# Kernel tuning notes

Hardware: AMD Instinct MI355X
Metric: run time of the kernel (lower is better)

## Reference

```python
import jax, jax.numpy as jnp
import numpy as np
import math

S, B, D, H = 2048, 4, 1024, 16
DH = D // H

def setup_inputs() -> dict:
    key = jax.random.key(0)
    ks = jax.random.split(key, 6)
    x = jax.random.normal(ks[0], (S, B, D), dtype=jnp.float32)
    # causal additive mask (finite large negative for numerical safety)
    i = jnp.arange(S)
    attn_mask = jnp.where(i[None, :] > i[:, None], jnp.float32(-1e9), jnp.float32(0.0))
    beta = jnp.zeros((H,), dtype=jnp.float32)  # per-head log-scale, init 0 -> exp=1
    xav = math.sqrt(6.0 / (D + D))  # xavier_uniform bound
    Wq = jax.random.uniform(ks[1], (D, D), minval=-xav, maxval=xav, dtype=jnp.float32)
    Wk = jax.random.uniform(ks[2], (D, D), minval=-xav, maxval=xav, dtype=jnp.float32)
    Wv = jax.random.uniform(ks[3], (D, D), minval=-xav, maxval=xav, dtype=jnp.float32)
    Wo = jax.random.uniform(ks[4], (D, D), minval=-xav, maxval=xav, dtype=jnp.float32)
    z = jnp.zeros((D,), dtype=jnp.float32)
    return {"x": x, "attn_mask": attn_mask, "beta": beta,
            "Wq": Wq, "bq": z, "Wk": Wk, "bk": z, "Wv": Wv, "bv": z, "Wo": Wo, "bo": z}

def reference(x, attn_mask, beta, Wq, bq, Wk, bk, Wv, bv, Wo, bo):
    s, b, d = x.shape
    h, dh = H, DH
    q = x @ Wq.T + bq  # (s, b, d)
    k = x @ Wk.T + bk
    v = x @ Wv.T + bv
    # attn_sink: append zero key/value token, pad mask with a zero column
    k = jnp.concatenate([k, jnp.zeros((1, b, d), k.dtype)], axis=0)  # (s+1, b, d)
    v = jnp.concatenate([v, jnp.zeros((1, b, d), v.dtype)], axis=0)
    mask = jnp.pad(attn_mask, ((0, 0), (0, 1)))  # (s, s+1)
    t = s + 1
    # split heads: (seq, b, h, dh) -> (b, h, seq, dh)
    qh = q.reshape(s, b, h, dh).transpose(1, 2, 0, 3)
    kh = k.reshape(t, b, h, dh).transpose(1, 2, 0, 3)
    vh = v.reshape(t, b, h, dh).transpose(1, 2, 0, 3)
    scale = (jnp.exp(beta) * math.sqrt(dh))[None, :, None, None]
    qh = qh / scale
    scores = jnp.einsum('bhsd,bhtd->bhst', qh, kh) + mask[None, None]
    w = jax.nn.softmax(scores, axis=-1)
    out = jnp.einsum('bhst,bhtd->bhsd', w, vh)  # (b, h, s, dh)
    out = out.transpose(2, 0, 1, 3).reshape(s, b, d)
    return out @ Wo.T + bo
```

## Files before the change

kernel.cpp:

```cpp
#include <hip/hip_runtime.h>
#include <hip/hip_bf16.h>
#include <math.h>

#define S_LEN   2048
#define BATCH   4
#define DMODEL  1024
#define NHEAD   16
#define DHEAD   64
#define MROWS   (S_LEN * BATCH)

typedef __bf16 bf16;
typedef __bf16 bf16x8 __attribute__((ext_vector_type(8)));
typedef __bf16 bf16x4 __attribute__((ext_vector_type(4)));
typedef short  short4_t __attribute__((ext_vector_type(4)));
typedef float  f32x4  __attribute__((ext_vector_type(4)));

#define LOG2E 1.4426950408889634f

#define AS1C(p) (const __attribute__((address_space(1))) void*)(p)
#define AS3(p)  (__attribute__((address_space(3))) void*)(p)


__global__ __launch_bounds__(256) void cast_bf16(const float* __restrict__ in,
                                                 bf16* __restrict__ out, int n8) {
    int i = blockIdx.x * 256 + threadIdx.x;
    if (i >= n8) return;
    const float4* p = (const float4*)in;
    float4 a = p[i * 2], b = p[i * 2 + 1];
    bf16x8 o;
    o[0] = (bf16)a.x; o[1] = (bf16)a.y; o[2] = (bf16)a.z; o[3] = (bf16)a.w;
    o[4] = (bf16)b.x; o[5] = (bf16)b.y; o[6] = (bf16)b.z; o[7] = (bf16)b.w;
    *(bf16x8*)(out + (size_t)i * 8) = o;
}

__global__ __launch_bounds__(256) void cast3_bf16(const float* __restrict__ w0,
                                                  const float* __restrict__ w1,
                                                  const float* __restrict__ w2,
                                                  bf16* __restrict__ out) {
    const int seg = blockIdx.y;
    const float* in = (seg == 0) ? w0 : (seg == 1) ? w1 : w2;
    int i = blockIdx.x * 256 + threadIdx.x;
    const float4* p = (const float4*)in;
    float4 a = p[i * 2], b = p[i * 2 + 1];
    bf16x8 o;
    o[0] = (bf16)a.x; o[1] = (bf16)a.y; o[2] = (bf16)a.z; o[3] = (bf16)a.w;
    o[4] = (bf16)b.x; o[5] = (bf16)b.y; o[6] = (bf16)b.z; o[7] = (bf16)b.w;
    *(bf16x8*)(out + (size_t)seg * DMODEL * DMODEL + (size_t)i * 8) = o;
}

__global__ __launch_bounds__(256, 2) void qkv_gemm(const bf16* __restrict__ A,
                                                   const bf16* __restrict__ W,
                                                   const float* __restrict__ bq,
                                                   const float* __restrict__ bk,
                                                   const float* __restrict__ bv,
                                                   const float* __restrict__ beta,
                                                   bf16* __restrict__ Qo,
                                                   bf16* __restrict__ Kp,
                                                   bf16* __restrict__ Vp) {
    constexpr int BK = 32;
    constexpr int NTILES = DMODEL / BK;
    __shared__ __align__(16) bf16 sA[3][256 * BK];
    __shared__ __align__(16) bf16 sB[3][128 * BK];

    const int t    = threadIdx.x;
    const int lane = t & 63;
    const int wave = t >> 6;
    const int wr   = wave >> 1;
    const int wc   = wave & 1;
    const int lq   = lane & 15;
    const int lg   = lane >> 4;
    const int bn   = blockIdx.x * 128;
    const int bm   = blockIdx.y * 256;

    const int schunk = (lane & 3) ^ ((lane >> 3) & 3);
    const bf16* ApS = A + (size_t)(bm + wave * 64 + (lane >> 2)) * DMODEL + schunk * 8;
    const bf16* WpS = W + (size_t)(bn + wave * 32 + (lane >> 2)) * DMODEL + schunk * 8;
    const int koff = (lg ^ ((lq >> 1) & 3)) * 8;

    f32x4 acc[8][4] = {};

#define QSTAGE(si_, ko_)                                                                              \
    __builtin_amdgcn_global_load_lds(AS1C(ApS + (ko_)),               AS3(&sA[si_][(wave*64 +  0)*BK]), 16,0,0); \
    __builtin_amdgcn_global_load_lds(AS1C(ApS + 16*DMODEL + (ko_)),   AS3(&sA[si_][(wave*64 + 16)*BK]), 16,0,0); \
    __builtin_amdgcn_global_load_lds(AS1C(ApS + 32*DMODEL + (ko_)),   AS3(&sA[si_][(wave*64 + 32)*BK]), 16,0,0); \
    __builtin_amdgcn_global_load_lds(AS1C(ApS + 48*DMODEL + (ko_)),   AS3(&sA[si_][(wave*64 + 48)*BK]), 16,0,0); \
    __builtin_amdgcn_global_load_lds(AS1C(WpS + (ko_)),               AS3(&sB[si_][(wave*32 +  0)*BK]), 16,0,0); \
    __builtin_amdgcn_global_load_lds(AS1C(WpS + 16*DMODEL + (ko_)),   AS3(&sB[si_][(wave*32 + 16)*BK]), 16,0,0);

    QSTAGE(0, 0)
    QSTAGE(1, BK)
    asm volatile("s_waitcnt vmcnt(6)\n\ts_barrier" ::: "memory");

    int bi = 0, si = 2, st = 2;
    for (int tt = 0; tt < NTILES; ++tt) {
        QSTAGE(si, (size_t)st * BK)
        const bf16* At = sA[bi];
        const bf16* Bt = sB[bi];
        bf16x8 bfr[4];
#pragma unroll
        for (int nt = 0; nt < 4; nt++)
            bfr[nt] = *(const bf16x8*)&Bt[(wc * 64 + nt * 16 + lq) * BK + koff];
        bf16x8 af[4];
#pragma unroll
        for (int mt = 0; mt < 4; mt++)
            af[mt] = *(const bf16x8*)&At[(wr * 128 + mt * 16 + lq) * BK + koff];
        __builtin_amdgcn_s_setprio(1);
#pragma unroll
        for (int mt = 0; mt < 4; mt++)
#pragma unroll
            for (int nt = 0; nt < 4; nt++)
                acc[mt][nt] = __builtin_amdgcn_mfma_f32_16x16x32_bf16(af[mt], bfr[nt], acc[mt][nt], 0, 0, 0);
        __builtin_amdgcn_s_setprio(0);
#pragma unroll
        for (int mt = 0; mt < 4; mt++)
            af[mt] = *(const bf16x8*)&At[(wr * 128 + (mt + 4) * 16 + lq) * BK + koff];
        __builtin_amdgcn_s_setprio(1);
#pragma unroll
        for (int mt = 0; mt < 4; mt++)
#pragma unroll
            for (int nt = 0; nt < 4; nt++)
                acc[mt + 4][nt] = __builtin_amdgcn_mfma_f32_16x16x32_bf16(af[mt], bfr[nt], acc[mt + 4][nt], 0, 0, 0);
        __builtin_amdgcn_s_setprio(0);
        asm volatile("s_waitcnt vmcnt(6)\n\ts_barrier" ::: "memory");
        bi = (bi == 2) ? 0 : bi + 1;
        si = (si == 2) ? 0 : si + 1;
        st = (st == NTILES - 1) ? 0 : st + 1;
    }
#undef QSTAGE

    const int seg = blockIdx.x >> 3;
    const int bnl = (blockIdx.x & 7) * 128;
    const float* bias = (seg == 0) ? bq : (seg == 1) ? bk : bv;

    if (seg == 0) {
#pragma unroll
        for (int nt = 0; nt < 4; nt++) {
            const int col = bnl + wc * 64 + nt * 16 + lq;
            const float bvv = bias[col];
            const float sc = LOG2E / (__expf(beta[col >> 6]) * 8.0f);
#pragma unroll
            for (int mt = 0; mt < 8; mt++) {
                const int row = bm + wr * 128 + mt * 16 + lg * 4;
#pragma unroll
                for (int r = 0; r < 4; r++) {
                    float v = (acc[mt][nt][r] + bvv) * sc;
                    Qo[(size_t)(row + r) * DMODEL + col] = (bf16)v;
                }
            }
        }
    } else {
        bf16* out = (seg == 1) ? Kp : Vp;
#pragma unroll
        for (int mt = 0; mt < 8; mt++) {
            const int F   = bm + wr * 128 + mt * 16;
            const int S0X = F >> 2;
            const int T   = S0X >> 4;
            const int sl  = (S0X & 15) + lg;
#pragma unroll
            for (int nt = 0; nt < 4; nt++) {
                const int col = bnl + wc * 64 + nt * 16 + lq;
                const int h   = col >> 6;
                const int dh  = col & 63;
                const float bvv = bias[col];
#pragma unroll
                for (int r = 0; r < 4; r++) {
                    float v = acc[mt][nt][r] + bvv;
                    size_t addr;
                    if (seg == 1) {
                        addr = ((size_t)((r * 16 + h) * 128 + T)) * 1024
                             + (dh >> 5) * 512
                             + (sl + 16 * ((dh >> 3) & 3)) * 8
                             + (dh & 7);
                    } else {
                        addr = ((size_t)((r * 16 + h) * 128 + T)) * 1024
                             + (dh >> 4) * 256 + ((dh & 15) + 16 * (sl >> 2)) * 4
                             + (sl & 3);
                    }
                    out[addr] = (bf16)v;
                }
            }
        }
    }
}

__global__ __launch_bounds__(256, 2) void gemm_out(const bf16* __restrict__ A,
                                                   const bf16* __restrict__ W,
                                                   const float* __restrict__ bias,
                                                   float* __restrict__ C) {
    constexpr int BK = 32;
    constexpr int NTILES = DMODEL / BK;
    __shared__ __align__(16) bf16 sA[3][128 * BK];
    __shared__ __align__(16) bf16 sB[3][128 * BK];

    const int t    = threadIdx.x;
    const int lane = t & 63;
    const int wave = t >> 6;
    const int wr   = wave >> 1;
    const int wc   = wave & 1;
    const int lq   = lane & 15;
    const int lg   = lane >> 4;
    const int bn   = blockIdx.x * 128;
    const int bm   = blockIdx.y * 128;

    const int schunk = (lane & 3) ^ ((lane >> 3) & 3);
    const bf16* ApS = A + (size_t)(bm + wave * 32 + (lane >> 2)) * DMODEL + schunk * 8;
    const bf16* WpS = W + (size_t)(bn + wave * 32 + (lane >> 2)) * DMODEL + schunk * 8;
    const int koff = (lg ^ ((lq >> 1) & 3)) * 8;

    f32x4 acc[4][4] = {};

#define OSTAGE(si_, ko_)                                                                              \
    __builtin_amdgcn_global_load_lds(AS1C(ApS + (ko_)),               AS3(&sA[si_][(wave*32 +  0)*BK]), 16,0,0); \
    __builtin_amdgcn_global_load_lds(AS1C(ApS + 16*DMODEL + (ko_)),   AS3(&sA[si_][(wave*32 + 16)*BK]), 16,0,0); \
    __builtin_amdgcn_global_load_lds(AS1C(WpS + (ko_)),               AS3(&sB[si_][(wave*32 +  0)*BK]), 16,0,0); \
    __builtin_amdgcn_global_load_lds(AS1C(WpS + 16*DMODEL + (ko_)),   AS3(&sB[si_][(wave*32 + 16)*BK]), 16,0,0);

    OSTAGE(0, 0)
    OSTAGE(1, BK)
    asm volatile("s_waitcnt vmcnt(4)\n\ts_barrier" ::: "memory");

    int bi = 0, si = 2, st = 2;
    for (int tt = 0; tt < NTILES; ++tt) {
        OSTAGE(si, (size_t)st * BK)
        const bf16* At = sA[bi];
        const bf16* Bt = sB[bi];
        bf16x8 bfr[4], af[4];
#pragma unroll
        for (int nt = 0; nt < 4; nt++)
            bfr[nt] = *(const bf16x8*)&Bt[(wc * 64 + nt * 16 + lq) * BK + koff];
#pragma unroll
        for (int mt = 0; mt < 4; mt++)
            af[mt] = *(const bf16x8*)&At[(wr * 64 + mt * 16 + lq) * BK + koff];
        __builtin_amdgcn_s_setprio(1);
#pragma unroll
        for (int mt = 0; mt < 4; mt++)
#pragma unroll
            for (int nt = 0; nt < 4; nt++)
                acc[mt][nt] = __builtin_amdgcn_mfma_f32_16x16x32_bf16(af[mt], bfr[nt], acc[mt][nt], 0, 0, 0);
        __builtin_amdgcn_s_setprio(0);
        asm volatile("s_waitcnt vmcnt(4)\n\ts_barrier" ::: "memory");
        bi = (bi == 2) ? 0 : bi + 1;
        si = (si == 2) ? 0 : si + 1;
        st = (st == NTILES - 1) ? 0 : st + 1;
    }
#undef OSTAGE

#pragma unroll
    for (int nt = 0; nt < 4; nt++) {
        const int col = bn + wc * 64 + nt * 16 + lq;
        const float bvv = bias[col];
#pragma unroll
        for (int mt = 0; mt < 4; mt++) {
            const int row = bm + wr * 64 + mt * 16 + lg * 4;
#pragma unroll
            for (int r = 0; r < 4; r++)
                C[(size_t)(row + r) * DMODEL + col] = acc[mt][nt][r] + bvv;
        }
    }
}

__global__ __launch_bounds__(256, 3) void attn_kernel(const bf16* __restrict__ Q,
                                                      const bf16* __restrict__ Kp,
                                                      const bf16* __restrict__ Vp,
                                                      bf16* __restrict__ O) {
    __shared__ __align__(16) float sO[64 * 65];
    __shared__ __align__(16) float sL[256];

    const int t    = threadIdx.x;
    const int lane = t & 63;
    const int wave = t >> 6;
    const int lq = lane & 15;
    const int lg = lane >> 4;

    const int bid = (int)blockIdx.x + 32 * ((int)blockIdx.y + 16 * (int)blockIdx.z);
    const int swz = (bid & 7) * 256 + (bid >> 3);
    const int qi  = 31 - (swz & 31);
    const int h   = (swz >> 5) & 15;
    const int b   = swz >> 9;
    const int qb  = qi * 64;

    bf16x8 qf[4][2];
#pragma unroll
    for (int nt = 0; nt < 4; nt++)
#pragma unroll
        for (int kc = 0; kc < 2; kc++)
            qf[nt][kc] = *(const bf16x8*)
                &Q[((size_t)(qb + nt * 16 + lq) * BATCH + b) * DMODEL + h * DHEAD + kc * 32 + lg * 8];

    f32x4 o_acc[4][4] = {};
    float l_lane[4] = {0.f, 0.f, 0.f, 0.f};

    const bf16* Kb = Kp + (size_t)(b * NHEAD + h) * 131072;
    const bf16* Vb = Vp + (size_t)(b * NHEAD + h) * 131072;

    bf16x8 kc0 = *(const bf16x8*)(Kb + (size_t)wave * 1024 + lane * 8);
    bf16x8 kc1 = *(const bf16x8*)(Kb + (size_t)wave * 1024 + 512 + lane * 8);
    bf16x4 vc0 = *(const bf16x4*)(Vb + (size_t)wave * 1024 +   0 + lane * 4);
    bf16x4 vc1 = *(const bf16x4*)(Vb + (size_t)wave * 1024 + 256 + lane * 4);
    bf16x4 vc2 = *(const bf16x4*)(Vb + (size_t)wave * 1024 + 512 + lane * 4);
    bf16x4 vc3 = *(const bf16x4*)(Vb + (size_t)wave * 1024 + 768 + lane * 4);

    for (int kt = 0; kt <= qi; kt++) {
        const int tn = ((kt < qi) ? (kt + 1) : 0) * 4 + wave;
        const bf16* Kn = Kb + (size_t)tn * 1024;
        const bf16* Vn = Vb + (size_t)tn * 1024;
        bf16x8 kn0 = *(const bf16x8*)(Kn + lane * 8);
        bf16x8 kn1 = *(const bf16x8*)(Kn + 512 + lane * 8);
        bf16x4 vn0 = *(const bf16x4*)(Vn +   0 + lane * 4);
        bf16x4 vn1 = *(const bf16x4*)(Vn + 256 + lane * 4);
        bf16x4 vn2 = *(const bf16x4*)(Vn + 512 + lane * 4);
        bf16x4 vn3 = *(const bf16x4*)(Vn + 768 + lane * 4);

        f32x4 st[4];
        __builtin_amdgcn_s_setprio(1);
#pragma unroll
        for (int nt = 0; nt < 4; nt++) {
            f32x4 a = {};
            a = __builtin_amdgcn_mfma_f32_16x16x32_bf16(kc0, qf[nt][0], a, 0, 0, 0);
            a = __builtin_amdgcn_mfma_f32_16x16x32_bf16(kc1, qf[nt][1], a, 0, 0, 0);
            st[nt] = a;
        }
        __builtin_amdgcn_s_setprio(0);

        if (kt == qi) {
#pragma unroll
            for (int nt = 0; nt < 4; nt++)
#pragma unroll
                for (int r = 0; r < 4; r++)
                    if (wave * 16 + lg * 4 + r > nt * 16 + lq) st[nt][r] = -1e30f;
        }

        short4_t pf[4];
#pragma unroll
        for (int nt = 0; nt < 4; nt++) {
            float p0 = __builtin_amdgcn_exp2f(st[nt][0]);
            float p1 = __builtin_amdgcn_exp2f(st[nt][1]);
            float p2 = __builtin_amdgcn_exp2f(st[nt][2]);
            float p3 = __builtin_amdgcn_exp2f(st[nt][3]);
            l_lane[nt] += (p0 + p1) + (p2 + p3);
            bf16x4 pv;
            pv[0] = (bf16)p0; pv[1] = (bf16)p1; pv[2] = (bf16)p2; pv[3] = (bf16)p3;
            pf[nt] = __builtin_bit_cast(short4_t, pv);
        }

        short4_t va0 = __builtin_bit_cast(short4_t, vc0);
        short4_t va1 = __builtin_bit_cast(short4_t, vc1);
        short4_t va2 = __builtin_bit_cast(short4_t, vc2);
        short4_t va3 = __builtin_bit_cast(short4_t, vc3);
        __builtin_amdgcn_s_setprio(1);
#pragma unroll
        for (int nt = 0; nt < 4; nt++) {
            o_acc[0][nt] = __builtin_amdgcn_mfma_f32_16x16x16bf16_1k(va0, pf[nt], o_acc[0][nt], 0, 0, 0);
            o_acc[1][nt] = __builtin_amdgcn_mfma_f32_16x16x16bf16_1k(va1, pf[nt], o_acc[1][nt], 0, 0, 0);
            o_acc[2][nt] = __builtin_amdgcn_mfma_f32_16x16x16bf16_1k(va2, pf[nt], o_acc[2][nt], 0, 0, 0);
            o_acc[3][nt] = __builtin_amdgcn_mfma_f32_16x16x16bf16_1k(va3, pf[nt], o_acc[3][nt], 0, 0, 0);
        }
        __builtin_amdgcn_s_setprio(0);

        kc0 = kn0; kc1 = kn1;
        vc0 = vn0; vc1 = vn1; vc2 = vn2; vc3 = vn3;
    }

#pragma unroll
    for (int nt = 0; nt < 4; nt++) {
        float v = l_lane[nt];
        v += __shfl_xor(v, 16);
        v += __shfl_xor(v, 32);
        if (lg == 0) sL[wave * 64 + nt * 16 + lq] = v;
    }

#pragma unroll
    for (int rd = 0; rd < 4; rd++) {
#pragma unroll
        for (int dtc = 0; dtc < 4; dtc++) {
            if (((wave + rd) & 3) == dtc) {
                if (rd == 0) {
#pragma unroll
                    for (int nt = 0; nt < 4; nt++)
#pragma unroll
                        for (int r = 0; r < 4; r++)
                            sO[(dtc * 16 + lg * 4 + r) * 65 + nt * 16 + lq] = o_acc[dtc][nt][r];
                } else {
#pragma unroll
                    for (int nt = 0; nt < 4; nt++)
#pragma unroll
                        for (int r = 0; r < 4; r++)
                            sO[(dtc * 16 + lg * 4 + r) * 65 + nt * 16 + lq] += o_acc[dtc][nt][r];
                }
            }
        }
        __syncthreads();
    }

    const int dt = wave;
    float rec[4];
#pragma unroll
    for (int nt = 0; nt < 4; nt++) {
        float lt = 1.0f + sL[nt * 16 + lq] + sL[64 + nt * 16 + lq]
                 + sL[128 + nt * 16 + lq] + sL[192 + nt * 16 + lq];
        rec[nt] = 1.0f / lt;
    }
#pragma unroll
    for (int nt = 0; nt < 4; nt++) {
        bf16x4 ov;
#pragma unroll
        for (int r = 0; r < 4; r++)
            ov[r] = (bf16)(sO[(dt * 16 + lg * 4 + r) * 65 + nt * 16 + lq] * rec[nt]);
        *(bf16x4*)&O[((size_t)(qb + nt * 16 + lq) * BATCH + b) * DMODEL + h * DHEAD + dt * 16 + lg * 4] = ov;
    }
}

extern "C" void kernel_launch(void* const* d_in, const int* in_sizes, int n_in,
                              void* d_out, int out_size, void* d_ws, size_t ws_size,
                              hipStream_t stream) {
    const float* x    = (const float*)d_in[0];
    const float* beta = (const float*)d_in[2];
    const float* Wq   = (const float*)d_in[3];
    const float* bq   = (const float*)d_in[4];
    const float* Wk   = (const float*)d_in[5];
    const float* bk   = (const float*)d_in[6];
    const float* Wv   = (const float*)d_in[7];
    const float* bv   = (const float*)d_in[8];
    const float* Wo   = (const float*)d_in[9];
    const float* bo   = (const float*)d_in[10];
    float* out = (float*)d_out;

    char* ws = (char*)d_ws;
    size_t off = 0;
    auto alloc = [&](size_t bytes) -> void* {
        void* p = ws + off;
        off += (bytes + 255) & ~(size_t)255;
        return p;
    };
    const size_t xbytes = (size_t)MROWS * DMODEL * sizeof(bf16);
    const size_t wbytes = (size_t)DMODEL * DMODEL * sizeof(bf16);
    bf16* xb   = (bf16*)alloc(xbytes);
    bf16* wqkv = (bf16*)alloc(3 * wbytes);
    bf16* wob  = (bf16*)alloc(wbytes);
    bf16* qws  = (bf16*)alloc(xbytes);
    bf16* kpb  = (bf16*)alloc(xbytes);
    bf16* vpb  = (bf16*)alloc(xbytes);
    bf16* aob  = (bf16*)alloc(xbytes);

    const int nx8 = MROWS * DMODEL / 8;
    const int nw8 = DMODEL * DMODEL / 8;
    cast_bf16<<<(nx8 + 255) / 256, 256, 0, stream>>>(x, xb, nx8);
    cast_bf16<<<(nw8 + 255) / 256, 256, 0, stream>>>(Wo, wob, nw8);
    dim3 c3grid(nw8 / 256, 3);
    cast3_bf16<<<c3grid, 256, 0, stream>>>(Wq, Wk, Wv, wqkv);

    dim3 qgrid(3 * DMODEL / 128, MROWS / 256);
    qkv_gemm<<<qgrid, 256, 0, stream>>>(xb, wqkv, bq, bk, bv, beta, qws, kpb, vpb);

    dim3 agrid(S_LEN / 64, NHEAD, BATCH);
    attn_kernel<<<agrid, 256, 0, stream>>>(qws, kpb, vpb, aob);

    dim3 ogrid(DMODEL / 128, MROWS / 128);
    gemm_out<<<ogrid, 256, 0, stream>>>(aob, wob, bo, out);
}
```

Baseline: 286.9 us.

## Enlarge QKV GEMM tile to 256x256 with 8 waves and interleaved staging

The QKV projection GEMM moves from 256-thread blocks with 256x128 tiles to 512-thread blocks with 256x256 tiles, one block per CU. Global-to-LDS loads for the next stage are split into four pieces and interleaved between four MFMA phases, with barriers in between, to spread memory traffic across the compute. Fragment reuse is arranged so each phase reloads only half of the A or B operands. This doubles LDS use for B and halves the grid, which may cut occupancy and add barrier overhead. The epilogue's column mapping is updated to match.

```diff
diff --git a/kernel.cpp b/kernel.cpp
--- a/kernel.cpp
+++ b/kernel.cpp
@@ -48,7 +48,7 @@
     *(bf16x8*)(out + (size_t)seg * DMODEL * DMODEL + (size_t)i * 8) = o;
 }
 
-__global__ __launch_bounds__(256, 2) void qkv_gemm(const bf16* __restrict__ A,
+__global__ __launch_bounds__(512, 1) void qkv_gemm(const bf16* __restrict__ A,
                                                    const bf16* __restrict__ W,
                                                    const float* __restrict__ bq,
                                                    const float* __restrict__ bk,
@@ -58,78 +58,109 @@
                                                    bf16* __restrict__ Kp,
                                                    bf16* __restrict__ Vp) {
     constexpr int BK = 32;
-    constexpr int NTILES = DMODEL / BK;
+    constexpr int NT = DMODEL / BK;
     __shared__ __align__(16) bf16 sA[3][256 * BK];
-    __shared__ __align__(16) bf16 sB[3][128 * BK];
+    __shared__ __align__(16) bf16 sB[3][256 * BK];
 
     const int t    = threadIdx.x;
     const int lane = t & 63;
     const int wave = t >> 6;
-    const int wr   = wave >> 1;
-    const int wc   = wave & 1;
+    const int wr   = wave >> 2;
+    const int wc   = wave & 3;
     const int lq   = lane & 15;
     const int lg   = lane >> 4;
-    const int bn   = blockIdx.x * 128;
+    const int bn   = blockIdx.x * 256;
     const int bm   = blockIdx.y * 256;
 
     const int schunk = (lane & 3) ^ ((lane >> 3) & 3);
-    const bf16* ApS = A + (size_t)(bm + wave * 64 + (lane >> 2)) * DMODEL + schunk * 8;
-    const bf16* WpS = W + (size_t)(bn + wave * 32 + (lane >> 2)) * DMODEL + schunk * 8;
+    const bf16* ApS = A + (size_t)(bm + wave * 16 + (lane >> 2)) * DMODEL + schunk * 8;
+    const bf16* WpS = W + (size_t)(bn + wave * 16 + (lane >> 2)) * DMODEL + schunk * 8;
     const int koff = (lg ^ ((lq >> 1) & 3)) * 8;
 
     f32x4 acc[8][4] = {};
 
-#define QSTAGE(si_, ko_)                                                                              \
-    __builtin_amdgcn_global_load_lds(AS1C(ApS + (ko_)),               AS3(&sA[si_][(wave*64 +  0)*BK]), 16,0,0); \
-    __builtin_amdgcn_global_load_lds(AS1C(ApS + 16*DMODEL + (ko_)),   AS3(&sA[si_][(wave*64 + 16)*BK]), 16,0,0); \
-    __builtin_amdgcn_global_load_lds(AS1C(ApS + 32*DMODEL + (ko_)),   AS3(&sA[si_][(wave*64 + 32)*BK]), 16,0,0); \
-    __builtin_amdgcn_global_load_lds(AS1C(ApS + 48*DMODEL + (ko_)),   AS3(&sA[si_][(wave*64 + 48)*BK]), 16,0,0); \
-    __builtin_amdgcn_global_load_lds(AS1C(WpS + (ko_)),               AS3(&sB[si_][(wave*32 +  0)*BK]), 16,0,0); \
-    __builtin_amdgcn_global_load_lds(AS1C(WpS + 16*DMODEL + (ko_)),   AS3(&sB[si_][(wave*32 + 16)*BK]), 16,0,0);
-
-    QSTAGE(0, 0)
-    QSTAGE(1, BK)
-    asm volatile("s_waitcnt vmcnt(6)\n\ts_barrier" ::: "memory");
+#define STG_A(si_, j_, st_) __builtin_amdgcn_global_load_lds(                            \
+        AS1C(ApS + (size_t)(j_) * 128 * DMODEL + (size_t)(st_) * BK),                    \
+        AS3(&sA[si_][((j_) * 128 + wave * 16) * BK]), 16, 0, 0);
+#define STG_B(si_, j_, st_) __builtin_amdgcn_global_load_lds(                            \
+        AS1C(WpS + (size_t)(j_) * 128 * DMODEL + (size_t)(st_) * BK),                    \
+        AS3(&sB[si_][((j_) * 128 + wave * 16) * BK]), 16, 0, 0);
+
+    STG_A(0, 0, 0) STG_A(0, 1, 0) STG_B(0, 0, 0) STG_B(0, 1, 0)
+    STG_A(1, 0, 1) STG_A(1, 1, 1) STG_B(1, 0, 1) STG_B(1, 1, 1)
+    asm volatile("s_waitcnt vmcnt(4)\n\ts_barrier" ::: "memory");
 
     int bi = 0, si = 2, st = 2;
-    for (int tt = 0; tt < NTILES; ++tt) {
-        QSTAGE(si, (size_t)st * BK)
+    for (int tt = 0; tt < NT; ++tt) {
         const bf16* At = sA[bi];
         const bf16* Bt = sB[bi];
-        bf16x8 bfr[4];
-#pragma unroll
-        for (int nt = 0; nt < 4; nt++)
-            bfr[nt] = *(const bf16x8*)&Bt[(wc * 64 + nt * 16 + lq) * BK + koff];
-        bf16x8 af[4];
-#pragma unroll
-        for (int mt = 0; mt < 4; mt++)
-            af[mt] = *(const bf16x8*)&At[(wr * 128 + mt * 16 + lq) * BK + koff];
-        __builtin_amdgcn_s_setprio(1);
-#pragma unroll
-        for (int mt = 0; mt < 4; mt++)
-#pragma unroll
-            for (int nt = 0; nt < 4; nt++)
-                acc[mt][nt] = __builtin_amdgcn_mfma_f32_16x16x32_bf16(af[mt], bfr[nt], acc[mt][nt], 0, 0, 0);
-        __builtin_amdgcn_s_setprio(0);
-#pragma unroll
-        for (int mt = 0; mt < 4; mt++)
-            af[mt] = *(const bf16x8*)&At[(wr * 128 + (mt + 4) * 16 + lq) * BK + koff];
-        __builtin_amdgcn_s_setprio(1);
-#pragma unroll
-        for (int mt = 0; mt < 4; mt++)
-#pragma unroll
-            for (int nt = 0; nt < 4; nt++)
-                acc[mt + 4][nt] = __builtin_amdgcn_mfma_f32_16x16x32_bf16(af[mt], bfr[nt], acc[mt + 4][nt], 0, 0, 0);
-        __builtin_amdgcn_s_setprio(0);
-        asm volatile("s_waitcnt vmcnt(6)\n\ts_barrier" ::: "memory");
+        bf16x8 af[4], bfr[2];
+
+#pragma unroll
+        for (int mf = 0; mf < 4; mf++)
+            af[mf] = *(const bf16x8*)&At[(wr * 128 + mf * 16 + lq) * BK + koff];
+        bfr[0] = *(const bf16x8*)&Bt[(wc * 64 +  0 + lq) * BK + koff];
+        bfr[1] = *(const bf16x8*)&Bt[(wc * 64 + 16 + lq) * BK + koff];
+        STG_A(si, 0, st)
+        __builtin_amdgcn_s_barrier();
+        __builtin_amdgcn_s_setprio(1);
+#pragma unroll
+        for (int mf = 0; mf < 4; mf++) {
+            acc[mf][0] = __builtin_amdgcn_mfma_f32_16x16x32_bf16(af[mf], bfr[0], acc[mf][0], 0, 0, 0);
+            acc[mf][1] = __builtin_amdgcn_mfma_f32_16x16x32_bf16(af[mf], bfr[1], acc[mf][1], 0, 0, 0);
+        }
+        __builtin_amdgcn_s_setprio(0);
+        __builtin_amdgcn_s_barrier();
+
+        bfr[0] = *(const bf16x8*)&Bt[(wc * 64 + 32 + lq) * BK + koff];
+        bfr[1] = *(const bf16x8*)&Bt[(wc * 64 + 48 + lq) * BK + koff];
+        STG_A(si, 1, st)
+        __builtin_amdgcn_s_barrier();
+        __builtin_amdgcn_s_setprio(1);
+#pragma unroll
+        for (int mf = 0; mf < 4; mf++) {
+            acc[mf][2] = __builtin_amdgcn_mfma_f32_16x16x32_bf16(af[mf], bfr[0], acc[mf][2], 0, 0, 0);
+            acc[mf][3] = __builtin_amdgcn_mfma_f32_16x16x32_bf16(af[mf], bfr[1], acc[mf][3], 0, 0, 0);
+        }
+        __builtin_amdgcn_s_setprio(0);
+        __builtin_amdgcn_s_barrier();
+
+#pragma unroll
+        for (int mf = 0; mf < 4; mf++)
+            af[mf] = *(const bf16x8*)&At[(wr * 128 + (mf + 4) * 16 + lq) * BK + koff];
+        STG_B(si, 0, st)
+        __builtin_amdgcn_s_barrier();
+        __builtin_amdgcn_s_setprio(1);
+#pragma unroll
+        for (int mf = 0; mf < 4; mf++) {
+            acc[mf + 4][2] = __builtin_amdgcn_mfma_f32_16x16x32_bf16(af[mf], bfr[0], acc[mf + 4][2], 0, 0, 0);
+            acc[mf + 4][3] = __builtin_amdgcn_mfma_f32_16x16x32_bf16(af[mf], bfr[1], acc[mf + 4][3], 0, 0, 0);
+        }
+        __builtin_amdgcn_s_setprio(0);
+        __builtin_amdgcn_s_barrier();
+
+        bfr[0] = *(const bf16x8*)&Bt[(wc * 64 +  0 + lq) * BK + koff];
+        bfr[1] = *(const bf16x8*)&Bt[(wc * 64 + 16 + lq) * BK + koff];
+        STG_B(si, 1, st)
+        __builtin_amdgcn_s_barrier();
+        __builtin_amdgcn_s_setprio(1);
+#pragma unroll
+        for (int mf = 0; mf < 4; mf++) {
+            acc[mf + 4][0] = __builtin_amdgcn_mfma_f32_16x16x32_bf16(af[mf], bfr[0], acc[mf + 4][0], 0, 0, 0);
+            acc[mf + 4][1] = __builtin_amdgcn_mfma_f32_16x16x32_bf16(af[mf], bfr[1], acc[mf + 4][1], 0, 0, 0);
+        }
+        __builtin_amdgcn_s_setprio(0);
+
+        asm volatile("s_waitcnt vmcnt(4)\n\ts_barrier" ::: "memory");
         bi = (bi == 2) ? 0 : bi + 1;
         si = (si == 2) ? 0 : si + 1;
-        st = (st == NTILES - 1) ? 0 : st + 1;
-    }
-#undef QSTAGE
-
-    const int seg = blockIdx.x >> 3;
-    const int bnl = (blockIdx.x & 7) * 128;
+        st = (st == NT - 1) ? 0 : st + 1;
+    }
+#undef STG_A
+#undef STG_B
+
+    const int seg = blockIdx.x >> 2;
+    const int bnl = (blockIdx.x & 3) * 256;
     const float* bias = (seg == 0) ? bq : (seg == 1) ? bk : bv;
 
     if (seg == 0) {
@@ -449,8 +480,8 @@
     dim3 c3grid(nw8 / 256, 3);
     cast3_bf16<<<c3grid, 256, 0, stream>>>(Wq, Wk, Wv, wqkv);
 
-    dim3 qgrid(3 * DMODEL / 128, MROWS / 256);
-    qkv_gemm<<<qgrid, 256, 0, stream>>>(xb, wqkv, bq, bk, bv, beta, qws, kpb, vpb);
+    dim3 qgrid(3 * DMODEL / 256, MROWS / 256);
+    qkv_gemm<<<qgrid, 512, 0, stream>>>(xb, wqkv, bq, bk, bv, beta, qws, kpb, vpb);
 
     dim3 agrid(S_LEN / 64, NHEAD, BATCH);
     attn_kernel<<<agrid, 256, 0, stream>>>(qws, kpb, vpb, aob);
```

Result: slower. 294.5 us (+2.7%).
